# Performance work log

Hardware: AMD Instinct MI355X
Metric: run time of the kernel (lower is better)

Reference implementation:

```python
import jax, jax.numpy as jnp
import numpy as np

TOLERANCE = 0.01  # init kwarg


def setup_inputs() -> dict:
    key = jax.random.key(0)
    k1, k2 = jax.random.split(key)
    B, N = 64, 2048
    logits = jax.random.normal(k1, (B, N), dtype=jnp.float32)
    labels = jax.random.uniform(k2, (B, N), dtype=jnp.float32)
    return {"logits": logits, "labels": labels}


def reference(logits, labels):
    # Original: for each row, sort labels descending; for every ordered pair
    # (high, low) in that order with |label_high - label_low| > tolerance,
    # accumulate log(sigmoid(logit_high - logit_low)); reduction='sum' per
    # row, then mean over the batch.
    # Vectorized equivalent: a pair contributes iff labels[a] - labels[b] > tol
    # (exactly one ordering per unordered pair, ties masked out).
    label_diff = labels[:, :, None] - labels[:, None, :]          # [B, N, N]
    mask = label_diff > TOLERANCE                                  # [B, N, N]
    logit_diff = logits[:, :, None] - logits[:, None, :]          # [B, N, N]
    log_sig = jax.nn.log_sigmoid(logit_diff)
    per_row = jnp.sum(jnp.where(mask, log_sig, 0.0), axis=(1, 2))  # [B]
    return jnp.mean(per_row)
```

## Files before the change

### kernel.cpp

```cpp
#include <hip/hip_runtime.h>
#include <math.h>


#define NN 2048
#define BB 64
#define TOLF 0.01f
#define BLK 256
#define NTILE 20
#define TILEBLKS (BB * NTILE)
#define SIDEBLKS (BB * 8)
#define WGRID (TILEBLKS + SIDEBLKS)
#define SWIN 448
#define LOG2E 1.4426950408889634f

__device__ float2 g_labs[BB][NN];
__device__ float  g_Es[BB][NN];
__device__ int    g_C[BB][NN];
__device__ float  g_part[TILEBLKS];
__device__ double g_partS[SIDEBLKS];

__global__ __launch_bounds__(BLK) void rank_pre(const float* __restrict__ logits,
                                                const float* __restrict__ labels) {
    __shared__ float2 sls[NN];
    __shared__ float  sEv[NN];
    __shared__ int    sC[NN];
    __shared__ int    cnt[100], pref[101], offs[100];
    __shared__ int    wtot;
    const int row = blockIdx.x, tid = threadIdx.x;
    const float* lg = logits + (size_t)row * NN;
    const float* lb = labels + (size_t)row * NN;

    for (int x = tid; x < 100; x += BLK) { cnt[x] = 0; offs[x] = 0; }
    __syncthreads();

    int   myb[8];
    float myla[8], mylg[8];
#pragma unroll
    for (int q = 0; q < 8; ++q) {
        int x = tid + q * BLK;
        myla[q] = lb[x];
        mylg[q] = lg[x];
        myb[q]  = min(99, (int)(myla[q] * 100.0f));
        atomicAdd(&cnt[myb[q]], 1);
    }
    __syncthreads();
    {
        int v = (tid < 100) ? cnt[tid] : 0;
        int x = v;
#pragma unroll
        for (int o = 1; o < 64; o <<= 1) {
            int y = __shfl_up(x, o);
            if ((tid & 63) >= o) x += y;
        }
        if (tid == 63) wtot = x;
        __syncthreads();
        if (tid >= 64 && tid < 128) x += wtot;
        if (tid < 101) pref[tid] = x - v;
    }
    __syncthreads();
#pragma unroll
    for (int q = 0; q < 8; ++q) {
        int b = myb[q];
        int p = pref[b] + atomicAdd(&offs[b], 1);
        float s = mylg[q] * LOG2E;
        sls[p] = make_float2(myla[q], s);
        sEv[p] = __builtin_amdgcn_exp2f(s);
        sC[p]  = (b >= 1) ? pref[b - 1] : 0;
    }
    __syncthreads();
    for (int x = tid; x < NN; x += BLK) {
        g_labs[row][x] = sls[x];
        g_Es[row][x]   = sEv[x];
        g_C[row][x]    = sC[x];
    }
}

__global__ __launch_bounds__(BLK) void rank_work() {
    const int bid = blockIdx.x;
    if (bid < SIDEBLKS) {
        __shared__ float2 sLS[SWIN];
        __shared__ float  sE[SWIN];
        __shared__ int    sCs;
        __shared__ double sdw[4];
        const int row = bid >> 3;
        const int c0  = (bid & 7) << 8;
        const int tid = threadIdx.x;
        if (tid == 0) sCs = g_C[row][c0];
        __syncthreads();
        const int Cs  = sCs;
        const int len = c0 + 256 - Cs;
        for (int x = tid; x < len; x += BLK) {
            sLS[x] = g_labs[row][Cs + x];
            sE[x]  = g_Es[row][Cs + x];
        }
        __syncthreads();

        const int i    = c0 + tid;
        const int iloc = i - Cs;
        const float2 lsi = sLS[iloc];
        const float lai = lsi.x, si = lsi.y;
        const float Ei  = sE[iloc];
        const int wloc  = g_C[row][i] - Cs;

        float accL = 0.0f, accS = 0.0f;
        float p = 1.0f;
        int cnt8 = 0;
        for (int j = wloc; j < iloc; ++j) {
            float2 ls = sLS[j];
            float ld = lai - ls.x;
            bool valid = fabsf(ld) > TOLF;
            float term = valid ? (Ei + sE[j]) : 1.0f;
            p *= term;
            if (++cnt8 == 8) { accL += __builtin_amdgcn_logf(p); p = 1.0f; cnt8 = 0; }
            float sh = (ld > 0.0f) ? si : ls.y;
            accS -= valid ? sh : 0.0f;
        }
        accL += __builtin_amdgcn_logf(p);

        double acc = (double)accL + (double)accS;
        for (int off = 32; off > 0; off >>= 1) acc += __shfl_down(acc, off);
        if ((tid & 63) == 0) sdw[tid >> 6] = acc;
        __syncthreads();
        if (tid == 0) g_partS[bid] = sdw[0] + sdw[1] + sdw[2] + sdw[3];
    } else {
        __shared__ __align__(16) float swin[256];
        __shared__ float swave[4];
        const int tb = bid - SIDEBLKS;
        const int row = tb / NTILE;
        const int t = tb % NTILE;
        const int it = (t < 2) ? 0 : (t < 6) ? 1 : (t < 12) ? 2 : 3;
        const int jt = t - it * (it + 1);
        const int ibeg = it * 512, jbeg = jt * 256;

        float accL = 0.0f;
        const int Cmax = g_C[row][ibeg + 511];
        if (jbeg < Cmax) {
            for (int x = threadIdx.x; x < 64; x += BLK)
                ((float4*)swin)[x] = ((const float4*)&g_Es[row][jbeg])[x];
            __syncthreads();
            const int ia = ibeg + threadIdx.x;
            const int ib = ia + 256;
            const float invEa = __builtin_amdgcn_rcpf(g_Es[row][ia]);
            const float invEb = __builtin_amdgcn_rcpf(g_Es[row][ib]);
            int tripa = max(0, min(256, g_C[row][ia] - jbeg));
            int tripb = max(0, min(256, g_C[row][ib] - jbeg));
            const int m16a = tripa & ~15;
            const int m16b = tripb & ~15;

            for (int jj = 0; jj < m16a; jj += 16) {
                const float4* q = (const float4*)&swin[jj];
                float4 w0 = q[0], w1 = q[1], w2 = q[2], w3 = q[3];
                float pa0 = 1.0f, pa1 = 1.0f, pb0 = 1.0f, pb1 = 1.0f;
                pa0 = fmaf(w0.x * invEa, pa0, pa0); pb0 = fmaf(w0.x * invEb, pb0, pb0);
                pa0 = fmaf(w0.y * invEa, pa0, pa0); pb0 = fmaf(w0.y * invEb, pb0, pb0);
                pa0 = fmaf(w0.z * invEa, pa0, pa0); pb0 = fmaf(w0.z * invEb, pb0, pb0);
                pa0 = fmaf(w0.w * invEa, pa0, pa0); pb0 = fmaf(w0.w * invEb, pb0, pb0);
                pa1 = fmaf(w1.x * invEa, pa1, pa1); pb1 = fmaf(w1.x * invEb, pb1, pb1);
                pa1 = fmaf(w1.y * invEa, pa1, pa1); pb1 = fmaf(w1.y * invEb, pb1, pb1);
                pa1 = fmaf(w1.z * invEa, pa1, pa1); pb1 = fmaf(w1.z * invEb, pb1, pb1);
                pa1 = fmaf(w1.w * invEa, pa1, pa1); pb1 = fmaf(w1.w * invEb, pb1, pb1);
                pa0 = fmaf(w2.x * invEa, pa0, pa0); pb0 = fmaf(w2.x * invEb, pb0, pb0);
                pa0 = fmaf(w2.y * invEa, pa0, pa0); pb0 = fmaf(w2.y * invEb, pb0, pb0);
                pa0 = fmaf(w2.z * invEa, pa0, pa0); pb0 = fmaf(w2.z * invEb, pb0, pb0);
                pa0 = fmaf(w2.w * invEa, pa0, pa0); pb0 = fmaf(w2.w * invEb, pb0, pb0);
                pa1 = fmaf(w3.x * invEa, pa1, pa1); pb1 = fmaf(w3.x * invEb, pb1, pb1);
                pa1 = fmaf(w3.y * invEa, pa1, pa1); pb1 = fmaf(w3.y * invEb, pb1, pb1);
                pa1 = fmaf(w3.z * invEa, pa1, pa1); pb1 = fmaf(w3.z * invEb, pb1, pb1);
                pa1 = fmaf(w3.w * invEa, pa1, pa1); pb1 = fmaf(w3.w * invEb, pb1, pb1);
                accL += __builtin_amdgcn_logf(pa0) + __builtin_amdgcn_logf(pa1)
                      + __builtin_amdgcn_logf(pb0) + __builtin_amdgcn_logf(pb1);
            }
            for (int jj = m16a; jj < m16b; jj += 16) {
                const float4* q = (const float4*)&swin[jj];
                float4 w0 = q[0], w1 = q[1], w2 = q[2], w3 = q[3];
                float pb0 = 1.0f, pb1 = 1.0f;
                pb0 = fmaf(w0.x * invEb, pb0, pb0);
                pb0 = fmaf(w0.y * invEb, pb0, pb0);
                pb0 = fmaf(w0.z * invEb, pb0, pb0);
                pb0 = fmaf(w0.w * invEb, pb0, pb0);
                pb1 = fmaf(w1.x * invEb, pb1, pb1);
                pb1 = fmaf(w1.y * invEb, pb1, pb1);
                pb1 = fmaf(w1.z * invEb, pb1, pb1);
                pb1 = fmaf(w1.w * invEb, pb1, pb1);
                pb0 = fmaf(w2.x * invEb, pb0, pb0);
                pb0 = fmaf(w2.y * invEb, pb0, pb0);
                pb0 = fmaf(w2.z * invEb, pb0, pb0);
                pb0 = fmaf(w2.w * invEb, pb0, pb0);
                pb1 = fmaf(w3.x * invEb, pb1, pb1);
                pb1 = fmaf(w3.y * invEb, pb1, pb1);
                pb1 = fmaf(w3.z * invEb, pb1, pb1);
                pb1 = fmaf(w3.w * invEb, pb1, pb1);
                accL += __builtin_amdgcn_logf(pb0) + __builtin_amdgcn_logf(pb1);
            }
            if (m16a < tripa) {
                float p0 = 1.0f, p1 = 1.0f;
#pragma unroll
                for (int u = 0; u < 8; ++u) {
                    float t0 = (m16a + u     < tripa) ? fmaf(swin[m16a + u],     invEa, 1.0f) : 1.0f;
                    float t1 = (m16a + 8 + u < tripa) ? fmaf(swin[m16a + 8 + u], invEa, 1.0f) : 1.0f;
                    p0 *= t0; p1 *= t1;
                }
                accL += __builtin_amdgcn_logf(p0) + __builtin_amdgcn_logf(p1);
            }
            if (m16b < tripb) {
                float p0 = 1.0f, p1 = 1.0f;
#pragma unroll
                for (int u = 0; u < 8; ++u) {
                    float t0 = (m16b + u     < tripb) ? fmaf(swin[m16b + u],     invEb, 1.0f) : 1.0f;
                    float t1 = (m16b + 8 + u < tripb) ? fmaf(swin[m16b + 8 + u], invEb, 1.0f) : 1.0f;
                    p0 *= t0; p1 *= t1;
                }
                accL += __builtin_amdgcn_logf(p0) + __builtin_amdgcn_logf(p1);
            }
        }
        for (int off = 32; off > 0; off >>= 1) accL += __shfl_down(accL, off);
        if ((threadIdx.x & 63) == 0) swave[threadIdx.x >> 6] = accL;
        __syncthreads();
        if (threadIdx.x == 0)
            g_part[tb] = swave[0] + swave[1] + swave[2] + swave[3];
    }
}

__global__ __launch_bounds__(BLK) void rank_final(float* __restrict__ out) {
    double acc = 0.0;
    for (int idx = threadIdx.x; idx < TILEBLKS; idx += BLK) acc += (double)g_part[idx];
    for (int idx = threadIdx.x; idx < SIDEBLKS; idx += BLK) acc += g_partS[idx];
    for (int off = 32; off > 0; off >>= 1) acc += __shfl_down(acc, off);
    __shared__ double sw[4];
    if ((threadIdx.x & 63) == 0) sw[threadIdx.x >> 6] = acc;
    __syncthreads();
    if (threadIdx.x == 0)
        out[0] = (float)((sw[0] + sw[1] + sw[2] + sw[3]) *
                         (-0.6931471805599453 / (double)BB));
}

extern "C" void kernel_launch(void* const* d_in, const int* in_sizes, int n_in,
                              void* d_out, int out_size, void* d_ws, size_t ws_size,
                              hipStream_t stream) {
    const float* logits = (const float*)d_in[0];
    const float* labels = (const float*)d_in[1];
    float* out = (float*)d_out;
    (void)in_sizes; (void)n_in; (void)out_size; (void)d_ws; (void)ws_size;

    rank_pre<<<BB, BLK, 0, stream>>>(logits, labels);
    rank_work<<<WGRID, BLK, 0, stream>>>();
    rank_final<<<1, BLK, 0, stream>>>(out);
}
```

Measured before the change: 27.13 us.

## Accumulate block sums via fixed-point atomics and reorder heavy tiles first

Each rank_work block now converts its partial sum to a 2^20-scaled integer and adds it atomically into a workspace counter. The final kernel then only rescales a single value instead of reducing 1792 partials. Preprocessing runs with 512 threads per row, and tile blocks are visited in reverse order so the larger lower-triangle tiles start first. This trades the reduction pass for contention on one global atomic and a fixed-point quantisation of the partial sums.

```diff
diff --git a/kernel.cpp b/kernel.cpp
--- a/kernel.cpp
+++ b/kernel.cpp
@@ -6,38 +6,40 @@
 #define BB 64
 #define TOLF 0.01f
 #define BLK 256
+#define BLKP 512
 #define NTILE 20
 #define TILEBLKS (BB * NTILE)
 #define SIDEBLKS (BB * 8)
 #define WGRID (TILEBLKS + SIDEBLKS)
 #define SWIN 448
 #define LOG2E 1.4426950408889634f
+#define FIXSCALE 1048576.0
 
 __device__ float2 g_labs[BB][NN];
 __device__ float  g_Es[BB][NN];
 __device__ int    g_C[BB][NN];
-__device__ float  g_part[TILEBLKS];
-__device__ double g_partS[SIDEBLKS];
-
-__global__ __launch_bounds__(BLK) void rank_pre(const float* __restrict__ logits,
-                                                const float* __restrict__ labels) {
+
+__global__ __launch_bounds__(BLKP) void rank_pre(const float* __restrict__ logits,
+                                                 const float* __restrict__ labels,
+                                                 unsigned long long* __restrict__ ws) {
     __shared__ float2 sls[NN];
     __shared__ float  sEv[NN];
     __shared__ int    sC[NN];
     __shared__ int    cnt[100], pref[101], offs[100];
     __shared__ int    wtot;
     const int row = blockIdx.x, tid = threadIdx.x;
+    if (row == 0 && tid == 0) ws[0] = 0ULL;
     const float* lg = logits + (size_t)row * NN;
     const float* lb = labels + (size_t)row * NN;
 
-    for (int x = tid; x < 100; x += BLK) { cnt[x] = 0; offs[x] = 0; }
-    __syncthreads();
-
-    int   myb[8];
-    float myla[8], mylg[8];
-#pragma unroll
-    for (int q = 0; q < 8; ++q) {
-        int x = tid + q * BLK;
+    for (int x = tid; x < 100; x += BLKP) { cnt[x] = 0; offs[x] = 0; }
+    __syncthreads();
+
+    int   myb[4];
+    float myla[4], mylg[4];
+#pragma unroll
+    for (int q = 0; q < 4; ++q) {
+        int x = tid + q * BLKP;
         myla[q] = lb[x];
         mylg[q] = lg[x];
         myb[q]  = min(99, (int)(myla[q] * 100.0f));
@@ -59,7 +61,7 @@
     }
     __syncthreads();
 #pragma unroll
-    for (int q = 0; q < 8; ++q) {
+    for (int q = 0; q < 4; ++q) {
         int b = myb[q];
         int p = pref[b] + atomicAdd(&offs[b], 1);
         float s = mylg[q] * LOG2E;
@@ -68,15 +70,17 @@
         sC[p]  = (b >= 1) ? pref[b - 1] : 0;
     }
     __syncthreads();
-    for (int x = tid; x < NN; x += BLK) {
+    for (int x = tid; x < NN; x += BLKP) {
         g_labs[row][x] = sls[x];
         g_Es[row][x]   = sEv[x];
         g_C[row][x]    = sC[x];
     }
 }
 
-__global__ __launch_bounds__(BLK) void rank_work() {
+__global__ __launch_bounds__(BLK) void rank_work(unsigned long long* __restrict__ ws) {
     const int bid = blockIdx.x;
+    double blockv = 0.0;
+
     if (bid < SIDEBLKS) {
         __shared__ float2 sLS[SWIN];
         __shared__ float  sE[SWIN];
@@ -121,13 +125,13 @@
         for (int off = 32; off > 0; off >>= 1) acc += __shfl_down(acc, off);
         if ((tid & 63) == 0) sdw[tid >> 6] = acc;
         __syncthreads();
-        if (tid == 0) g_partS[bid] = sdw[0] + sdw[1] + sdw[2] + sdw[3];
+        if (tid == 0) blockv = sdw[0] + sdw[1] + sdw[2] + sdw[3];
     } else {
         __shared__ __align__(16) float swin[256];
         __shared__ float swave[4];
         const int tb = bid - SIDEBLKS;
         const int row = tb / NTILE;
-        const int t = tb % NTILE;
+        const int t = (NTILE - 1) - (tb % NTILE);
         const int it = (t < 2) ? 0 : (t < 6) ? 1 : (t < 12) ? 2 : 3;
         const int jt = t - it * (it + 1);
         const int ibeg = it * 512, jbeg = jt * 256;
@@ -213,25 +217,27 @@
                 accL += __builtin_amdgcn_logf(p0) + __builtin_amdgcn_logf(p1);
             }
         }
-        for (int off = 32; off > 0; off >>= 1) accL += __shfl_down(accL, off);
-        if ((threadIdx.x & 63) == 0) swave[threadIdx.x >> 6] = accL;
+        float v = accL;
+        for (int off = 32; off > 0; off >>= 1) v += __shfl_down(v, off);
+        if ((threadIdx.x & 63) == 0) swave[threadIdx.x >> 6] = v;
         __syncthreads();
         if (threadIdx.x == 0)
-            g_part[tb] = swave[0] + swave[1] + swave[2] + swave[3];
-    }
-}
-
-__global__ __launch_bounds__(BLK) void rank_final(float* __restrict__ out) {
-    double acc = 0.0;
-    for (int idx = threadIdx.x; idx < TILEBLKS; idx += BLK) acc += (double)g_part[idx];
-    for (int idx = threadIdx.x; idx < SIDEBLKS; idx += BLK) acc += g_partS[idx];
-    for (int off = 32; off > 0; off >>= 1) acc += __shfl_down(acc, off);
-    __shared__ double sw[4];
-    if ((threadIdx.x & 63) == 0) sw[threadIdx.x >> 6] = acc;
-    __syncthreads();
-    if (threadIdx.x == 0)
-        out[0] = (float)((sw[0] + sw[1] + sw[2] + sw[3]) *
+            blockv = (double)(swave[0] + swave[1] + swave[2] + swave[3]);
+    }
+
+    if (threadIdx.x == 0) {
+        long long q = llrint(blockv * FIXSCALE);
+        atomicAdd(ws, (unsigned long long)q);
+    }
+}
+
+__global__ __launch_bounds__(64) void rank_final(float* __restrict__ out,
+                                                 const unsigned long long* __restrict__ ws) {
+    if (threadIdx.x == 0) {
+        long long tot = (long long)ws[0];
+        out[0] = (float)((double)tot * (1.0 / FIXSCALE) *
                          (-0.6931471805599453 / (double)BB));
+    }
 }
 
 extern "C" void kernel_launch(void* const* d_in, const int* in_sizes, int n_in,
@@ -240,9 +246,10 @@
     const float* logits = (const float*)d_in[0];
     const float* labels = (const float*)d_in[1];
     float* out = (float*)d_out;
-    (void)in_sizes; (void)n_in; (void)out_size; (void)d_ws; (void)ws_size;
-
-    rank_pre<<<BB, BLK, 0, stream>>>(logits, labels);
-    rank_work<<<WGRID, BLK, 0, stream>>>();
-    rank_final<<<1, BLK, 0, stream>>>(out);
-}
+    unsigned long long* ws = (unsigned long long*)d_ws;
+    (void)in_sizes; (void)n_in; (void)out_size; (void)ws_size;
+
+    rank_pre<<<BB, BLKP, 0, stream>>>(logits, labels, ws);
+    rank_work<<<WGRID, BLK, 0, stream>>>(ws);
+    rank_final<<<1, 64, 0, stream>>>(out, ws);
+}
```

New measurement: 38.44 us. 41.7% more time.

## Pack per-element label, logit, exp and bucket start into one float4 array

Applied to the files above, without the earlier changes.

Merges the three separate global arrays (label/scaled-logit pair, exp value, bucket start index) into a single float4-per-element array, so each consumer does one 16-byte load instead of several. The preprocessing kernel now runs with 512 threads per row and uses per-wave bucket histograms, which reduces LDS atomic contention and gives a deterministic per-wave offset layout. The tile path now reads the exp window with strided float4 loads, taking only the z component, which wastes bandwidth compared with the earlier contiguous float4 loads.

```diff
diff --git a/kernel.cpp b/kernel.cpp
--- a/kernel.cpp
+++ b/kernel.cpp
@@ -6,6 +6,7 @@
 #define BB 64
 #define TOLF 0.01f
 #define BLK 256
+#define BLKP 512
 #define NTILE 20
 #define TILEBLKS (BB * NTILE)
 #define SIDEBLKS (BB * 8)
@@ -13,39 +14,48 @@
 #define SWIN 448
 #define LOG2E 1.4426950408889634f
 
-__device__ float2 g_labs[BB][NN];
-__device__ float  g_Es[BB][NN];
-__device__ int    g_C[BB][NN];
+__device__ float4 g_pack[BB][NN];
 __device__ float  g_part[TILEBLKS];
 __device__ double g_partS[SIDEBLKS];
 
-__global__ __launch_bounds__(BLK) void rank_pre(const float* __restrict__ logits,
-                                                const float* __restrict__ labels) {
-    __shared__ float2 sls[NN];
-    __shared__ float  sEv[NN];
-    __shared__ int    sC[NN];
-    __shared__ int    cnt[100], pref[101], offs[100];
-    __shared__ int    wtot;
+__global__ __launch_bounds__(BLKP) void rank_pre(const float* __restrict__ logits,
+                                                 const float* __restrict__ labels) {
+    __shared__ float4 spk[NN];
+    __shared__ int cnt[8][100];
+    __shared__ int offs[8][100];
+    __shared__ int tot[100];
+    __shared__ int pref[101];
+    __shared__ int wtot;
     const int row = blockIdx.x, tid = threadIdx.x;
+    const int wv = tid >> 6;
     const float* lg = logits + (size_t)row * NN;
     const float* lb = labels + (size_t)row * NN;
 
-    for (int x = tid; x < 100; x += BLK) { cnt[x] = 0; offs[x] = 0; }
-    __syncthreads();
-
-    int   myb[8];
-    float myla[8], mylg[8];
-#pragma unroll
-    for (int q = 0; q < 8; ++q) {
-        int x = tid + q * BLK;
+    for (int x = tid; x < 800; x += BLKP) ((int*)cnt)[x] = 0;
+    __syncthreads();
+
+    int   myb[4];
+    float myla[4], mylg[4];
+#pragma unroll
+    for (int q = 0; q < 4; ++q) {
+        int x = tid + q * BLKP;
         myla[q] = lb[x];
         mylg[q] = lg[x];
         myb[q]  = min(99, (int)(myla[q] * 100.0f));
-        atomicAdd(&cnt[myb[q]], 1);
-    }
-    __syncthreads();
+        atomicAdd(&cnt[wv][myb[q]], 1);
+    }
+    __syncthreads();
+
+    if (tid < 100) {
+        int run = 0;
+#pragma unroll
+        for (int w = 0; w < 8; ++w) { offs[w][tid] = run; run += cnt[w][tid]; }
+        tot[tid] = run;
+    }
+    __syncthreads();
+
     {
-        int v = (tid < 100) ? cnt[tid] : 0;
+        int v = (tid < 100) ? tot[tid] : 0;
         int x = v;
 #pragma unroll
         for (int o = 1; o < 64; o <<= 1) {
@@ -58,21 +68,19 @@
         if (tid < 101) pref[tid] = x - v;
     }
     __syncthreads();
-#pragma unroll
-    for (int q = 0; q < 8; ++q) {
+
+#pragma unroll
+    for (int q = 0; q < 4; ++q) {
         int b = myb[q];
-        int p = pref[b] + atomicAdd(&offs[b], 1);
+        int p = pref[b] + atomicAdd(&offs[wv][b], 1);
         float s = mylg[q] * LOG2E;
-        sls[p] = make_float2(myla[q], s);
-        sEv[p] = __builtin_amdgcn_exp2f(s);
-        sC[p]  = (b >= 1) ? pref[b - 1] : 0;
-    }
-    __syncthreads();
-    for (int x = tid; x < NN; x += BLK) {
-        g_labs[row][x] = sls[x];
-        g_Es[row][x]   = sEv[x];
-        g_C[row][x]    = sC[x];
-    }
+        spk[p] = make_float4(myla[q], s, __builtin_amdgcn_exp2f(s),
+                             __int_as_float((b >= 1) ? pref[b - 1] : 0));
+    }
+    __syncthreads();
+
+    for (int x = tid; x < NN; x += BLKP)
+        g_pack[row][x] = spk[x];
 }
 
 __global__ __launch_bounds__(BLK) void rank_work() {
@@ -85,22 +93,23 @@
         const int row = bid >> 3;
         const int c0  = (bid & 7) << 8;
         const int tid = threadIdx.x;
-        if (tid == 0) sCs = g_C[row][c0];
+        if (tid == 0) sCs = __float_as_int(g_pack[row][c0].w);
         __syncthreads();
         const int Cs  = sCs;
         const int len = c0 + 256 - Cs;
         for (int x = tid; x < len; x += BLK) {
-            sLS[x] = g_labs[row][Cs + x];
-            sE[x]  = g_Es[row][Cs + x];
+            float4 v = g_pack[row][Cs + x];
+            sLS[x] = make_float2(v.x, v.y);
+            sE[x]  = v.z;
         }
         __syncthreads();
 
         const int i    = c0 + tid;
-        const int iloc = i - Cs;
-        const float2 lsi = sLS[iloc];
-        const float lai = lsi.x, si = lsi.y;
-        const float Ei  = sE[iloc];
-        const int wloc  = g_C[row][i] - Cs;
+        const float4 pki = g_pack[row][i];
+        const float lai = pki.x, si = pki.y;
+        const float Ei  = pki.z;
+        const int wloc  = __float_as_int(pki.w) - Cs;
+        const int iloc  = i - Cs;
 
         float accL = 0.0f, accS = 0.0f;
         float p = 1.0f;
@@ -133,17 +142,18 @@
         const int ibeg = it * 512, jbeg = jt * 256;
 
         float accL = 0.0f;
-        const int Cmax = g_C[row][ibeg + 511];
+        const int Cmax = __float_as_int(g_pack[row][ibeg + 511].w);
         if (jbeg < Cmax) {
-            for (int x = threadIdx.x; x < 64; x += BLK)
-                ((float4*)swin)[x] = ((const float4*)&g_Es[row][jbeg])[x];
+            swin[threadIdx.x] = g_pack[row][jbeg + threadIdx.x].z;
             __syncthreads();
             const int ia = ibeg + threadIdx.x;
             const int ib = ia + 256;
-            const float invEa = __builtin_amdgcn_rcpf(g_Es[row][ia]);
-            const float invEb = __builtin_amdgcn_rcpf(g_Es[row][ib]);
-            int tripa = max(0, min(256, g_C[row][ia] - jbeg));
-            int tripb = max(0, min(256, g_C[row][ib] - jbeg));
+            const float4 pka = g_pack[row][ia];
+            const float4 pkb = g_pack[row][ib];
+            const float invEa = __builtin_amdgcn_rcpf(pka.z);
+            const float invEb = __builtin_amdgcn_rcpf(pkb.z);
+            int tripa = max(0, min(256, __float_as_int(pka.w) - jbeg));
+            int tripb = max(0, min(256, __float_as_int(pkb.w) - jbeg));
             const int m16a = tripa & ~15;
             const int m16b = tripb & ~15;
 
@@ -242,7 +252,7 @@
     float* out = (float*)d_out;
     (void)in_sizes; (void)n_in; (void)out_size; (void)d_ws; (void)ws_size;
 
-    rank_pre<<<BB, BLK, 0, stream>>>(logits, labels);
+    rank_pre<<<BB, BLKP, 0, stream>>>(logits, labels);
     rank_work<<<WGRID, BLK, 0, stream>>>();
     rank_final<<<1, BLK, 0, stream>>>(out);
 }
```

Result: slower. 27.84 us (+2.6%).

## Split bucket-sort preprocessing into histogram and wide global-atomic scatter kernels

Applied to the files above, without the earlier changes.

The single per-row preprocessing kernel (64 blocks) is replaced by a histogram/prefix kernel that writes bucket offsets to global memory and a scatter kernel spread over 512 blocks. The scatter uses global atomics on per-row bucket counters to place each element. The aim is more parallelism in the preprocessing stage, which previously ran on only 64 workgroups. In exchange it adds a kernel launch, global atomic contention, and uncoalesced scattered global writes instead of staging through shared memory.

```diff
diff --git a/kernel.cpp b/kernel.cpp
--- a/kernel.cpp
+++ b/kernel.cpp
@@ -16,33 +16,20 @@
 __device__ float2 g_labs[BB][NN];
 __device__ float  g_Es[BB][NN];
 __device__ int    g_C[BB][NN];
+__device__ int    g_pref[BB][101];
+__device__ int    g_offs[BB][100];
 __device__ float  g_part[TILEBLKS];
 __device__ double g_partS[SIDEBLKS];
 
-__global__ __launch_bounds__(BLK) void rank_pre(const float* __restrict__ logits,
-                                                const float* __restrict__ labels) {
-    __shared__ float2 sls[NN];
-    __shared__ float  sEv[NN];
-    __shared__ int    sC[NN];
-    __shared__ int    cnt[100], pref[101], offs[100];
-    __shared__ int    wtot;
+__global__ __launch_bounds__(BLK) void rank_hist(const float* __restrict__ labels) {
+    __shared__ int cnt[100];
+    __shared__ int wtot;
     const int row = blockIdx.x, tid = threadIdx.x;
-    const float* lg = logits + (size_t)row * NN;
     const float* lb = labels + (size_t)row * NN;
-
-    for (int x = tid; x < 100; x += BLK) { cnt[x] = 0; offs[x] = 0; }
+    for (int x = tid; x < 100; x += BLK) cnt[x] = 0;
     __syncthreads();
-
-    int   myb[8];
-    float myla[8], mylg[8];
-#pragma unroll
-    for (int q = 0; q < 8; ++q) {
-        int x = tid + q * BLK;
-        myla[q] = lb[x];
-        mylg[q] = lg[x];
-        myb[q]  = min(99, (int)(myla[q] * 100.0f));
-        atomicAdd(&cnt[myb[q]], 1);
-    }
+    for (int x = tid; x < NN; x += BLK)
+        atomicAdd(&cnt[min(99, (int)(lb[x] * 100.0f))], 1);
     __syncthreads();
     {
         int v = (tid < 100) ? cnt[tid] : 0;
@@ -55,24 +42,27 @@
         if (tid == 63) wtot = x;
         __syncthreads();
         if (tid >= 64 && tid < 128) x += wtot;
-        if (tid < 101) pref[tid] = x - v;
+        if (tid < 101) {
+            int pr = x - v;
+            g_pref[row][tid] = pr;
+            if (tid < 100) g_offs[row][tid] = pr;
+        }
     }
-    __syncthreads();
-#pragma unroll
-    for (int q = 0; q < 8; ++q) {
-        int b = myb[q];
-        int p = pref[b] + atomicAdd(&offs[b], 1);
-        float s = mylg[q] * LOG2E;
-        sls[p] = make_float2(myla[q], s);
-        sEv[p] = __builtin_amdgcn_exp2f(s);
-        sC[p]  = (b >= 1) ? pref[b - 1] : 0;
-    }
-    __syncthreads();
-    for (int x = tid; x < NN; x += BLK) {
-        g_labs[row][x] = sls[x];
-        g_Es[row][x]   = sEv[x];
-        g_C[row][x]    = sC[x];
-    }
+}
+
+__global__ __launch_bounds__(BLK) void rank_scatter(const float* __restrict__ logits,
+                                                    const float* __restrict__ labels) {
+    const int bid = blockIdx.x;
+    const int row = bid >> 3;
+    const int x   = ((bid & 7) << 8) + threadIdx.x;
+    const float la  = labels[(size_t)row * NN + x];
+    const float lgx = logits[(size_t)row * NN + x];
+    const int b = min(99, (int)(la * 100.0f));
+    const int p = atomicAdd(&g_offs[row][b], 1);
+    const float s = lgx * LOG2E;
+    g_labs[row][p] = make_float2(la, s);
+    g_Es[row][p]   = __builtin_amdgcn_exp2f(s);
+    g_C[row][p]    = (b >= 1) ? g_pref[row][b - 1] : 0;
 }
 
 __global__ __launch_bounds__(BLK) void rank_work() {
@@ -242,7 +232,8 @@
     float* out = (float*)d_out;
     (void)in_sizes; (void)n_in; (void)out_size; (void)d_ws; (void)ws_size;
 
-    rank_pre<<<BB, BLK, 0, stream>>>(logits, labels);
+    rank_hist<<<BB, BLK, 0, stream>>>(labels);
+    rank_scatter<<<SIDEBLKS, BLK, 0, stream>>>(logits, labels);
     rank_work<<<WGRID, BLK, 0, stream>>>();
     rank_final<<<1, BLK, 0, stream>>>(out);
 }
```

Measured after the change: 34.84 us. 28.4% more time.
